# Kernel optimization log

Hardware: AMD Instinct MI355X
Metric: run time of the kernel (lower is better)

Reference implementation:

```python
import jax, jax.numpy as jnp
import numpy as np

N = 2_000_000
LAYER_DIMS = [6, 128, 48, 48, 48, 48, 48, 128, 3]  # 8 Linear layers


def setup_inputs() -> dict:
    key = jax.random.key(0)
    ks = jax.random.split(key, 2 + 2 * (len(LAYER_DIMS) - 1))
    inp = {
        "dimensions": jax.random.normal(ks[0], (N, 3), dtype=jnp.float32),
        "xyz": jax.random.normal(ks[1], (N, 3), dtype=jnp.float32),
    }
    # Kaiming-uniform-ish init like torch.nn.Linear defaults
    for i in range(len(LAYER_DIMS) - 1):
        fan_in, fan_out = LAYER_DIMS[i], LAYER_DIMS[i + 1]
        bound = 1.0 / np.sqrt(fan_in)
        inp[f"W{i+1}"] = jax.random.uniform(ks[2 + 2 * i], (fan_in, fan_out),
                                             minval=-bound, maxval=bound, dtype=jnp.float32)
        inp[f"b{i+1}"] = jax.random.uniform(ks[3 + 2 * i], (fan_out,),
                                             minval=-bound, maxval=bound, dtype=jnp.float32)
    return inp


def reference(dimensions, xyz,
              W1, b1, W2, b2, W3, b3, W4, b4,
              W5, b5, W6, b6, W7, b7, W8, b8) -> jnp.ndarray:
    x = jnp.concatenate([dimensions, xyz], axis=1)  # [N, 6]
    Ws = (W1, W2, W3, W4, W5, W6, W7)
    bs = (b1, b2, b3, b4, b5, b6, b7)
    for W, b in zip(Ws, bs):
        x = jax.nn.silu(x @ W + b)
    # final layer: Linear(128, 3) with Identity activation
    return x @ W8 + b8  # [N, 3]
```

## Files before the change

kernel.cpp:

```cpp
#include <hip/hip_runtime.h>

typedef __bf16 bf16x8 __attribute__((ext_vector_type(8)));
typedef __bf16 bf16x4 __attribute__((ext_vector_type(4)));
typedef float  f32x4  __attribute__((ext_vector_type(4)));

#define DEVFN static __device__ __forceinline__

DEVFN f32x4 mfma16(bf16x8 a, bf16x8 b, f32x4 c) {
  return __builtin_amdgcn_mfma_f32_16x16x32_bf16(a, b, c, 0, 0, 0);
}

DEVFN float silu_f(float x) {
  float e = __builtin_amdgcn_exp2f(x * -1.44269504f);
  return x * __builtin_amdgcn_rcpf(1.0f + e);
}

DEVFN void sbar() { __builtin_amdgcn_sched_barrier(0x7F); }

DEVFN bf16x8 bzero8() {
  bf16x8 v = {(__bf16)0.f,(__bf16)0.f,(__bf16)0.f,(__bf16)0.f,
              (__bf16)0.f,(__bf16)0.f,(__bf16)0.f,(__bf16)0.f};
  return v;
}
DEVFN f32x4 fzero4() { f32x4 v = {0.f,0.f,0.f,0.f}; return v; }

#define OFF_W2   0u
#define OFF_W3   12288u
#define OFF_W4   16896u
#define OFF_W5   21504u
#define OFF_W6   26112u
#define OFF_W7   30720u
#define OFF_BIAS 43008u
#define OFF_SCR  44992u
#define SCR_ROW    80u
#define SCR_RT     1280u
#define SCR_STRIDE 2560u
#define NWAVES   8
#define BLOCK    512
#define SMEM_TOTAL 65472u

DEVFN void init48(unsigned char* smem, unsigned base, const float* W, int Nout, int NT, int tid) {
  for (int t = tid; t < NT*512; t += BLOCK) {
    int i = t & 7, ln = (t >> 3) & 63, nt = t >> 9;
    int k = ((ln >> 4) << 3) + i;
    int n = (nt << 4) + (ln & 15);
    *(__bf16*)(smem + base + 2u*(unsigned)t) = (__bf16)W[k*Nout + n];
  }
  for (int t = tid; t < NT*256; t += BLOCK) {
    int i = t & 7, ln = (t >> 3) & 31, nt = t >> 8;
    int k = 32 + ((ln >> 4) << 3) + i;
    int n = (nt << 4) + (ln & 15);
    *(__bf16*)(smem + base + (unsigned)(NT*1024) + 2u*(unsigned)t) = (__bf16)W[k*Nout + n];
  }
}

DEVFN f32x4 biasFrag(const float* sB, int off, int nt, int g) {
  return *(const f32x4*)(sB + off + nt*16 + 4*g);
}

DEVFN void writeTile(unsigned char* sw, f32x4 t0, f32x4 t1, int slot, unsigned wBaseW) {
  bf16x4 p0, p1;
#pragma unroll
  for (int r = 0; r < 4; ++r) {
    p0[r] = (__bf16)silu_f(t0[r]);
    p1[r] = (__bf16)silu_f(t1[r]);
  }
  *(bf16x4*)(sw + wBaseW + (unsigned)slot*32u)           = p0;
  *(bf16x4*)(sw + SCR_RT + wBaseW + (unsigned)slot*32u)  = p1;
}

DEVFN void readA(const unsigned char* sw, unsigned aBase, bf16x8 (&af)[2]) {
  af[0] = *(const bf16x8*)(sw + aBase);
  af[1] = *(const bf16x8*)(sw + SCR_RT + aBase);
}

template<int NTO>
DEVFN void consumeFull(const unsigned char* smem, unsigned fragBase, unsigned bOff,
                       const bf16x8 (&af)[2], f32x4 (&acc)[2][NTO]) {
#pragma unroll
  for (int nt = 0; nt < NTO; ++nt) {
    bf16x8 w = *(const bf16x8*)(smem + fragBase + (unsigned)nt*1024u + bOff);
    acc[0][nt] = mfma16(w, af[0], acc[0][nt]);
    acc[1][nt] = mfma16(w, af[1], acc[1][nt]);
  }
}

template<int NTO>
DEVFN void consumeHalf(const unsigned char* smem, unsigned halfBase, unsigned hOff,
                       const bf16x8 (&af)[2], f32x4 (&acc)[2][NTO]) {
#pragma unroll
  for (int nt = 0; nt < NTO; ++nt) {
    bf16x8 w = *(const bf16x8*)(smem + halfBase + (unsigned)nt*512u + hOff);
    acc[0][nt] = mfma16(w, af[0], acc[0][nt]);
    acc[1][nt] = mfma16(w, af[1], acc[1][nt]);
  }
}

DEVFN void stream48(unsigned char* sw, unsigned char* smem,
                    unsigned wfragBase, const f32x4 (&accP)[2][3], f32x4 (&accO)[2][3],
                    unsigned wBaseW, unsigned aBase, unsigned bOff,
                    unsigned hOff, unsigned zOff) {
  bf16x8 af[2];
  sbar();
  writeTile(sw, accP[0][0], accP[1][0], 0, wBaseW);
  writeTile(sw, accP[0][1], accP[1][1], 1, wBaseW);
  sbar();
  readA(sw, aBase, af);
  consumeFull<3>(smem, wfragBase, bOff, af, accO);
  sbar();
  *(unsigned long long*)(sw + zOff)      = 0ull;
  *(unsigned long long*)(sw + zOff + 8u) = 0ull;
  writeTile(sw, accP[0][2], accP[1][2], 0, wBaseW);
  sbar();
  readA(sw, aBase, af);
  consumeHalf<3>(smem, wfragBase + 3u*1024u, hOff, af, accO);
}

DEVFN void loadIn(const float* __restrict__ dims, const float* __restrict__ xyz,
                  int grp, int lane, int N, float (&buf)[2][6]) {
#pragma unroll
  for (int rt = 0; rt < 2; ++rt)
#pragma unroll
    for (int j = 0; j < 6; ++j) buf[rt][j] = 0.f;
  if (lane < 16) {
#pragma unroll
    for (int rt = 0; rt < 2; ++rt) {
      int row = grp*32 + rt*16 + lane;
      if (row < N) {
        const float* dp = dims + (size_t)row*3u;
        const float* xp = xyz  + (size_t)row*3u;
        buf[rt][0] = dp[0]; buf[rt][1] = dp[1]; buf[rt][2] = dp[2];
        buf[rt][3] = xp[0]; buf[rt][4] = xp[1]; buf[rt][5] = xp[2];
      }
    }
  }
}

__global__ void __launch_bounds__(BLOCK, 4)
pinn_mlp_kernel(const float* __restrict__ dims, const float* __restrict__ xyz,
                const float* __restrict__ W1, const float* __restrict__ b1,
                const float* __restrict__ W2, const float* __restrict__ b2,
                const float* __restrict__ W3, const float* __restrict__ b3,
                const float* __restrict__ W4, const float* __restrict__ b4,
                const float* __restrict__ W5, const float* __restrict__ b5,
                const float* __restrict__ W6, const float* __restrict__ b6,
                const float* __restrict__ W7, const float* __restrict__ b7,
                const float* __restrict__ W8, const float* __restrict__ b8,
                float* __restrict__ out, int N) {
  __shared__ __align__(16) unsigned char smem[SMEM_TOTAL];
  const int tid  = threadIdx.x;
  const int lane = tid & 63;
  const int wave = tid >> 6;

  for (int t = tid; t < 6144; t += BLOCK) {
    int i = t & 7, ln = (t >> 3) & 63, f = t >> 9;
    int kt = f / 3, nt = f - kt*3;
    int k = kt*32 + ((ln >> 4) << 3) + i;
    int n = (nt << 4) + (ln & 15);
    *(__bf16*)(smem + OFF_W2 + 2u*(unsigned)t) = (__bf16)W2[k*48 + n];
  }
  init48(smem, OFF_W3, W3, 48, 3, tid);
  init48(smem, OFF_W4, W4, 48, 3, tid);
  init48(smem, OFF_W5, W5, 48, 3, tid);
  init48(smem, OFF_W6, W6, 48, 3, tid);
  init48(smem, OFF_W7, W7, 128, 8, tid);
  float* sB = (float*)(smem + OFF_BIAS);
  for (int t = tid; t < 496; t += BLOCK) {
    float v;
    if      (t < 128) v = b1[t];
    else if (t < 176) v = b2[t - 128];
    else if (t < 224) v = b3[t - 176];
    else if (t < 272) v = b4[t - 224];
    else if (t < 320) v = b5[t - 272];
    else if (t < 368) v = b6[t - 320];
    else              v = b7[t - 368];
    sB[t] = v;
  }

  bf16x8 w1f[8];
#pragma unroll
  for (int nt = 0; nt < 8; ++nt) w1f[nt] = bzero8();
  if (lane < 16) {
#pragma unroll
    for (int nt = 0; nt < 8; ++nt)
#pragma unroll
      for (int i = 0; i < 6; ++i)
        w1f[nt][i] = (__bf16)W1[i*128 + nt*16 + lane];
  }
  bf16x8 w8f[4];
#pragma unroll
  for (int kt = 0; kt < 4; ++kt) {
    w8f[kt] = bzero8();
    int n = lane & 15;
    if (n < 3) {
#pragma unroll
      for (int i = 0; i < 8; ++i) {
        int k = kt*32 + ((lane >> 4) << 3) + i;
        w8f[kt][i] = (__bf16)W8[k*3 + n];
      }
    }
  }

  __syncthreads();

  const int colId = lane & 15;
  const int g     = lane >> 4;
  unsigned char* sw = smem + OFF_SCR + (unsigned)wave * SCR_STRIDE;
  const unsigned aBase  = (unsigned)colId*SCR_ROW + (unsigned)g*16u;
  const unsigned wBaseW = (unsigned)colId*SCR_ROW + (unsigned)g*8u;
  const unsigned bOff   = (unsigned)lane*16u;
  const unsigned hOff   = (unsigned)(lane & 31)*16u;
  const unsigned zOff   = (unsigned)(lane >> 1)*SCR_ROW + 32u + (unsigned)(lane & 1)*16u;

  f32x4 b8v = fzero4();
  if (g == 0) { b8v[0] = b8[0]; b8v[1] = b8[1]; b8v[2] = b8[2]; }

  const int nGroups  = (N + 31) >> 5;
  const int gw0      = blockIdx.x*NWAVES + wave;
  const int gwStride = gridDim.x*NWAVES;

  float inC[2][6], inN[2][6];
  loadIn(dims, xyz, gw0, lane, N, inC);

  for (int grp = gw0; grp < nGroups; grp += gwStride) {
    const int base = grp * 32;

    bf16x8 a1[2] = {bzero8(), bzero8()};
    if (lane < 16) {
#pragma unroll
      for (int rt = 0; rt < 2; ++rt)
#pragma unroll
        for (int j = 0; j < 6; ++j) a1[rt][j] = (__bf16)inC[rt][j];
    }
    loadIn(dims, xyz, grp + gwStride, lane, N, inN);

    f32x4 accA[2][3], accB[2][3];
#pragma unroll
    for (int b = 0; b < 3; ++b) {
      f32x4 bi = biasFrag(sB, 128, b, g);
      accA[0][b] = bi; accA[1][b] = bi;
    }
#pragma unroll
    for (int kt = 0; kt < 4; ++kt) {
      sbar();
#pragma unroll
      for (int c = 0; c < 2; ++c) {
        int nt = 2*kt + c;
        f32x4 bi = biasFrag(sB, 0, nt, g);
        f32x4 t0 = mfma16(w1f[nt], a1[0], bi);
        f32x4 t1 = mfma16(w1f[nt], a1[1], bi);
        writeTile(sw, t0, t1, c, wBaseW);
      }
      sbar();
      bf16x8 af[2]; readA(sw, aBase, af);
      consumeFull<3>(smem, OFF_W2 + (unsigned)kt*3072u, bOff, af, accA);
    }

#pragma unroll
    for (int b = 0; b < 3; ++b) { f32x4 bi = biasFrag(sB, 176, b, g); accB[0][b] = bi; accB[1][b] = bi; }
    stream48(sw, smem, OFF_W3, accA, accB, wBaseW, aBase, bOff, hOff, zOff);
#pragma unroll
    for (int b = 0; b < 3; ++b) { f32x4 bi = biasFrag(sB, 224, b, g); accA[0][b] = bi; accA[1][b] = bi; }
    stream48(sw, smem, OFF_W4, accB, accA, wBaseW, aBase, bOff, hOff, zOff);
#pragma unroll
    for (int b = 0; b < 3; ++b) { f32x4 bi = biasFrag(sB, 272, b, g); accB[0][b] = bi; accB[1][b] = bi; }
    stream48(sw, smem, OFF_W5, accA, accB, wBaseW, aBase, bOff, hOff, zOff);
#pragma unroll
    for (int b = 0; b < 3; ++b) { f32x4 bi = biasFrag(sB, 320, b, g); accA[0][b] = bi; accA[1][b] = bi; }
    stream48(sw, smem, OFF_W6, accB, accA, wBaseW, aBase, bOff, hOff, zOff);

    sbar();
    writeTile(sw, accA[0][0], accA[1][0], 0, wBaseW);
    writeTile(sw, accA[0][1], accA[1][1], 1, wBaseW);
    sbar();
    bf16x8 af0[2]; readA(sw, aBase, af0);
    sbar();
    *(unsigned long long*)(sw + zOff)      = 0ull;
    *(unsigned long long*)(sw + zOff + 8u) = 0ull;
    writeTile(sw, accA[0][2], accA[1][2], 0, wBaseW);
    sbar();
    bf16x8 af1[2]; readA(sw, aBase, af1);

    f32x4 acc8[2] = {b8v, b8v};
#pragma unroll
    for (int kt = 0; kt < 4; ++kt) {
      sbar();
#pragma unroll
      for (int c = 0; c < 2; ++c) {
        int nt = 2*kt + c;
        bf16x8 wfull = *(const bf16x8*)(smem + OFF_W7 + (unsigned)nt*1024u + bOff);
        bf16x8 whalf = *(const bf16x8*)(smem + OFF_W7 + 8192u + (unsigned)nt*512u + hOff);
        f32x4 bi = biasFrag(sB, 368, nt, g);
        f32x4 t0 = mfma16(whalf, af1[0], mfma16(wfull, af0[0], bi));
        f32x4 t1 = mfma16(whalf, af1[1], mfma16(wfull, af0[1], bi));
        writeTile(sw, t0, t1, c, wBaseW);
      }
      sbar();
      bf16x8 af8[2]; readA(sw, aBase, af8);
      acc8[0] = mfma16(w8f[kt], af8[0], acc8[0]);
      acc8[1] = mfma16(w8f[kt], af8[1], acc8[1]);
    }

    if (g == 0) {
#pragma unroll
      for (int rt = 0; rt < 2; ++rt) {
        int row = base + rt*16 + colId;
        if (row < N) {
          size_t o = (size_t)row*3u;
          out[o+0] = acc8[rt][0];
          out[o+1] = acc8[rt][1];
          out[o+2] = acc8[rt][2];
        }
      }
    }

#pragma unroll
    for (int rt = 0; rt < 2; ++rt)
#pragma unroll
      for (int j = 0; j < 6; ++j) inC[rt][j] = inN[rt][j];
  }
}

extern "C" void kernel_launch(void* const* d_in, const int* in_sizes, int n_in,
                              void* d_out, int out_size, void* d_ws, size_t ws_size,
                              hipStream_t stream) {
  const float* dims = (const float*)d_in[0];
  const float* xyz  = (const float*)d_in[1];
  const float* W1 = (const float*)d_in[2];  const float* b1 = (const float*)d_in[3];
  const float* W2 = (const float*)d_in[4];  const float* b2 = (const float*)d_in[5];
  const float* W3 = (const float*)d_in[6];  const float* b3 = (const float*)d_in[7];
  const float* W4 = (const float*)d_in[8];  const float* b4 = (const float*)d_in[9];
  const float* W5 = (const float*)d_in[10]; const float* b5 = (const float*)d_in[11];
  const float* W6 = (const float*)d_in[12]; const float* b6 = (const float*)d_in[13];
  const float* W7 = (const float*)d_in[14]; const float* b7 = (const float*)d_in[15];
  const float* W8 = (const float*)d_in[16]; const float* b8 = (const float*)d_in[17];
  float* out = (float*)d_out;
  const int N = in_sizes[0] / 3;

  pinn_mlp_kernel<<<dim3(512), dim3(BLOCK), 0, stream>>>(
      dims, xyz, W1, b1, W2, b2, W3, b3, W4, b4, W5, b5, W6, b6, W7, b7, W8, b8,
      out, N);
}
```

Measured before the change: 298.2 us.

## Switch to 16x16x16 MFMA so layer outputs feed next layer in registers

Replaces the 16x16x32 bf16 MFMA with the 16x16x16 variant, whose output accumulator layout matches the B-operand layout. Each layer's silu output can then be packed directly into the next layer's input fragment without a round trip through per-wave LDS scratch. This removes the scratch buffer, its writes, reads, zero padding and scheduling barriers, and drops the 48-width padding to 64. In exchange it issues twice as many smaller MFMAs, each with half the K depth, and W1 now lives in LDS instead of registers.

```diff
diff --git a/kernel.cpp b/kernel.cpp
--- a/kernel.cpp
+++ b/kernel.cpp
@@ -1,13 +1,17 @@
 #include <hip/hip_runtime.h>
 
-typedef __bf16 bf16x8 __attribute__((ext_vector_type(8)));
 typedef __bf16 bf16x4 __attribute__((ext_vector_type(4)));
+typedef short  s16x4  __attribute__((ext_vector_type(4)));
 typedef float  f32x4  __attribute__((ext_vector_type(4)));
 
 #define DEVFN static __device__ __forceinline__
-
-DEVFN f32x4 mfma16(bf16x8 a, bf16x8 b, f32x4 c) {
-  return __builtin_amdgcn_mfma_f32_16x16x32_bf16(a, b, c, 0, 0, 0);
+#define BLOCK 512
+#define NWAVES 8
+
+DEVFN f32x4 mfma16(bf16x4 a, bf16x4 b, f32x4 c) {
+  s16x4 as = __builtin_bit_cast(s16x4, a);
+  s16x4 bs = __builtin_bit_cast(s16x4, b);
+  return __builtin_amdgcn_mfma_f32_16x16x16bf16_1k(as, bs, c, 0, 0, 0);
 }
 
 DEVFN float silu_f(float x) {
@@ -15,122 +19,88 @@
   return x * __builtin_amdgcn_rcpf(1.0f + e);
 }
 
-DEVFN void sbar() { __builtin_amdgcn_sched_barrier(0x7F); }
-
-DEVFN bf16x8 bzero8() {
-  bf16x8 v = {(__bf16)0.f,(__bf16)0.f,(__bf16)0.f,(__bf16)0.f,
-              (__bf16)0.f,(__bf16)0.f,(__bf16)0.f,(__bf16)0.f};
-  return v;
-}
-DEVFN f32x4 fzero4() { f32x4 v = {0.f,0.f,0.f,0.f}; return v; }
-
-#define OFF_W2   0u
-#define OFF_W3   12288u
-#define OFF_W4   16896u
-#define OFF_W5   21504u
-#define OFF_W6   26112u
-#define OFF_W7   30720u
-#define OFF_BIAS 43008u
-#define OFF_SCR  44992u
-#define SCR_ROW    80u
-#define SCR_RT     1280u
-#define SCR_STRIDE 2560u
-#define NWAVES   8
-#define BLOCK    512
-#define SMEM_TOTAL 65472u
-
-DEVFN void init48(unsigned char* smem, unsigned base, const float* W, int Nout, int NT, int tid) {
-  for (int t = tid; t < NT*512; t += BLOCK) {
-    int i = t & 7, ln = (t >> 3) & 63, nt = t >> 9;
-    int k = ((ln >> 4) << 3) + i;
-    int n = (nt << 4) + (ln & 15);
-    *(__bf16*)(smem + base + 2u*(unsigned)t) = (__bf16)W[k*Nout + n];
-  }
-  for (int t = tid; t < NT*256; t += BLOCK) {
-    int i = t & 7, ln = (t >> 3) & 31, nt = t >> 8;
-    int k = 32 + ((ln >> 4) << 3) + i;
-    int n = (nt << 4) + (ln & 15);
-    *(__bf16*)(smem + base + (unsigned)(NT*1024) + 2u*(unsigned)t) = (__bf16)W[k*Nout + n];
-  }
-}
-
-DEVFN f32x4 biasFrag(const float* sB, int off, int nt, int g) {
-  return *(const f32x4*)(sB + off + nt*16 + 4*g);
-}
-
-DEVFN void writeTile(unsigned char* sw, f32x4 t0, f32x4 t1, int slot, unsigned wBaseW) {
-  bf16x4 p0, p1;
-#pragma unroll
-  for (int r = 0; r < 4; ++r) {
-    p0[r] = (__bf16)silu_f(t0[r]);
-    p1[r] = (__bf16)silu_f(t1[r]);
-  }
-  *(bf16x4*)(sw + wBaseW + (unsigned)slot*32u)           = p0;
-  *(bf16x4*)(sw + SCR_RT + wBaseW + (unsigned)slot*32u)  = p1;
-}
-
-DEVFN void readA(const unsigned char* sw, unsigned aBase, bf16x8 (&af)[2]) {
-  af[0] = *(const bf16x8*)(sw + aBase);
-  af[1] = *(const bf16x8*)(sw + SCR_RT + aBase);
-}
-
-template<int NTO>
-DEVFN void consumeFull(const unsigned char* smem, unsigned fragBase, unsigned bOff,
-                       const bf16x8 (&af)[2], f32x4 (&acc)[2][NTO]) {
-#pragma unroll
-  for (int nt = 0; nt < NTO; ++nt) {
-    bf16x8 w = *(const bf16x8*)(smem + fragBase + (unsigned)nt*1024u + bOff);
-    acc[0][nt] = mfma16(w, af[0], acc[0][nt]);
-    acc[1][nt] = mfma16(w, af[1], acc[1][nt]);
-  }
-}
-
-template<int NTO>
-DEVFN void consumeHalf(const unsigned char* smem, unsigned halfBase, unsigned hOff,
-                       const bf16x8 (&af)[2], f32x4 (&acc)[2][NTO]) {
-#pragma unroll
-  for (int nt = 0; nt < NTO; ++nt) {
-    bf16x8 w = *(const bf16x8*)(smem + halfBase + (unsigned)nt*512u + hOff);
-    acc[0][nt] = mfma16(w, af[0], acc[0][nt]);
-    acc[1][nt] = mfma16(w, af[1], acc[1][nt]);
-  }
-}
-
-DEVFN void stream48(unsigned char* sw, unsigned char* smem,
-                    unsigned wfragBase, const f32x4 (&accP)[2][3], f32x4 (&accO)[2][3],
-                    unsigned wBaseW, unsigned aBase, unsigned bOff,
-                    unsigned hOff, unsigned zOff) {
-  bf16x8 af[2];
-  sbar();
-  writeTile(sw, accP[0][0], accP[1][0], 0, wBaseW);
-  writeTile(sw, accP[0][1], accP[1][1], 1, wBaseW);
-  sbar();
-  readA(sw, aBase, af);
-  consumeFull<3>(smem, wfragBase, bOff, af, accO);
-  sbar();
-  *(unsigned long long*)(sw + zOff)      = 0ull;
-  *(unsigned long long*)(sw + zOff + 8u) = 0ull;
-  writeTile(sw, accP[0][2], accP[1][2], 0, wBaseW);
-  sbar();
-  readA(sw, aBase, af);
-  consumeHalf<3>(smem, wfragBase + 3u*1024u, hOff, af, accO);
-}
-
-DEVFN void loadIn(const float* __restrict__ dims, const float* __restrict__ xyz,
-                  int grp, int lane, int N, float (&buf)[2][6]) {
-#pragma unroll
-  for (int rt = 0; rt < 2; ++rt)
-#pragma unroll
-    for (int j = 0; j < 6; ++j) buf[rt][j] = 0.f;
-  if (lane < 16) {
+DEVFN bf16x4 pksilu(f32x4 t) {
+  bf16x4 r;
+#pragma unroll
+  for (int j = 0; j < 4; ++j) r[j] = (__bf16)silu_f(t[j]);
+  return r;
+}
+
+#define OFF_W1   0u
+#define OFF_W2   4096u
+#define OFF_W3   16384u
+#define OFF_W4   20992u
+#define OFF_W5   25600u
+#define OFF_W6   30208u
+#define OFF_W7   34816u
+#define OFF_BIAS 47104u
+#define SMEM_TOTAL 49088u
+
+DEVFN void packW(unsigned char* smem, unsigned base, const float* W, int K, int N, int tid) {
+  int NT = N >> 4;
+  int total = (K >> 4) * NT * 256;
+  for (int t = tid; t < total; t += BLOCK) {
+    int i = t & 3, ln = (t >> 2) & 63, f = t >> 8;
+    int ks = f / NT, nt = f - ks * NT;
+    int k = 16 * ks + 4 * (ln >> 4) + i;
+    int n = 16 * nt + (ln & 15);
+    *(__bf16*)(smem + base + (unsigned)f * 512u + (unsigned)ln * 8u + (unsigned)i * 2u)
+        = (__bf16)W[k * N + n];
+  }
+}
+
+DEVFN f32x4 ldb(const float* sB, int off, int nt, int g) {
+  return *(const f32x4*)(sB + off + nt * 16 + 4 * g);
+}
+
+DEVFN bf16x4 ldw(const unsigned char* smem, unsigned addr) {
+  return *(const bf16x4*)(smem + addr);
+}
+
+DEVFN void layer33(const unsigned char* smem, unsigned wbase, const float* sB, int bOffL,
+                   unsigned wOff, int g, const bf16x4 (&xin)[2][3], bf16x4 (&xout)[2][3]) {
+  f32x4 acc[2][3];
+#pragma unroll
+  for (int nt = 0; nt < 3; ++nt) {
+    f32x4 bi = ldb(sB, bOffL, nt, g);
+    acc[0][nt] = bi; acc[1][nt] = bi;
+  }
+#pragma unroll
+  for (int ks = 0; ks < 3; ++ks)
+#pragma unroll
+    for (int nt = 0; nt < 3; ++nt) {
+      bf16x4 w = ldw(smem, wbase + (unsigned)(ks * 3 + nt) * 512u + wOff);
+      acc[0][nt] = mfma16(w, xin[0][ks], acc[0][nt]);
+      acc[1][nt] = mfma16(w, xin[1][ks], acc[1][nt]);
+    }
+#pragma unroll
+  for (int nt = 0; nt < 3; ++nt) {
+    xout[0][nt] = pksilu(acc[0][nt]);
+    xout[1][nt] = pksilu(acc[1][nt]);
+  }
+}
+
+DEVFN void loadIn6(const float* __restrict__ dims, const float* __restrict__ xyz,
+                   int grp, int g, int m, int N, float (&buf)[2][4]) {
+#pragma unroll
+  for (int rt = 0; rt < 2; ++rt) { buf[rt][0] = buf[rt][1] = buf[rt][2] = buf[rt][3] = 0.f; }
+  if (g == 0) {
 #pragma unroll
     for (int rt = 0; rt < 2; ++rt) {
-      int row = grp*32 + rt*16 + lane;
+      int row = grp * 32 + rt * 16 + m;
       if (row < N) {
-        const float* dp = dims + (size_t)row*3u;
-        const float* xp = xyz  + (size_t)row*3u;
+        const float* dp = dims + (size_t)row * 3u;
         buf[rt][0] = dp[0]; buf[rt][1] = dp[1]; buf[rt][2] = dp[2];
-        buf[rt][3] = xp[0]; buf[rt][4] = xp[1]; buf[rt][5] = xp[2];
+        buf[rt][3] = xyz[(size_t)row * 3u];
+      }
+    }
+  } else if (g == 1) {
+#pragma unroll
+    for (int rt = 0; rt < 2; ++rt) {
+      int row = grp * 32 + rt * 16 + m;
+      if (row < N) {
+        const float* xp = xyz + (size_t)row * 3u;
+        buf[rt][0] = xp[1]; buf[rt][1] = xp[2];
       }
     }
   }
@@ -151,20 +121,23 @@
   const int tid  = threadIdx.x;
   const int lane = tid & 63;
   const int wave = tid >> 6;
-
-  for (int t = tid; t < 6144; t += BLOCK) {
-    int i = t & 7, ln = (t >> 3) & 63, f = t >> 9;
-    int kt = f / 3, nt = f - kt*3;
-    int k = kt*32 + ((ln >> 4) << 3) + i;
-    int n = (nt << 4) + (ln & 15);
-    *(__bf16*)(smem + OFF_W2 + 2u*(unsigned)t) = (__bf16)W2[k*48 + n];
-  }
-  init48(smem, OFF_W3, W3, 48, 3, tid);
-  init48(smem, OFF_W4, W4, 48, 3, tid);
-  init48(smem, OFF_W5, W5, 48, 3, tid);
-  init48(smem, OFF_W6, W6, 48, 3, tid);
-  init48(smem, OFF_W7, W7, 128, 8, tid);
-  float* sB = (float*)(smem + OFF_BIAS);
+  const int m    = lane & 15;
+  const int g    = lane >> 4;
+
+  for (int t = tid; t < 2048; t += BLOCK) {
+    int i = t & 3, ln = (t >> 2) & 63, nt = t >> 8;
+    int k = 4 * (ln >> 4) + i;
+    int n = 16 * nt + (ln & 15);
+    float v = (k < 6) ? W1[k * 128 + n] : 0.f;
+    *(__bf16*)(smem + OFF_W1 + (unsigned)nt * 512u + (unsigned)ln * 8u + (unsigned)i * 2u) = (__bf16)v;
+  }
+  packW(smem, OFF_W2, W2, 128, 48, tid);
+  packW(smem, OFF_W3, W3, 48, 48, tid);
+  packW(smem, OFF_W4, W4, 48, 48, tid);
+  packW(smem, OFF_W5, W5, 48, 48, tid);
+  packW(smem, OFF_W6, W6, 48, 48, tid);
+  packW(smem, OFF_W7, W7, 48, 128, tid);
+  float* sBw = (float*)(smem + OFF_BIAS);
   for (int t = tid; t < 496; t += BLOCK) {
     float v;
     if      (t < 128) v = b1[t];
@@ -174,142 +147,124 @@
     else if (t < 320) v = b5[t - 272];
     else if (t < 368) v = b6[t - 320];
     else              v = b7[t - 368];
-    sB[t] = v;
-  }
-
-  bf16x8 w1f[8];
-#pragma unroll
-  for (int nt = 0; nt < 8; ++nt) w1f[nt] = bzero8();
-  if (lane < 16) {
-#pragma unroll
-    for (int nt = 0; nt < 8; ++nt)
-#pragma unroll
-      for (int i = 0; i < 6; ++i)
-        w1f[nt][i] = (__bf16)W1[i*128 + nt*16 + lane];
-  }
-  bf16x8 w8f[4];
-#pragma unroll
-  for (int kt = 0; kt < 4; ++kt) {
-    w8f[kt] = bzero8();
-    int n = lane & 15;
-    if (n < 3) {
-#pragma unroll
-      for (int i = 0; i < 8; ++i) {
-        int k = kt*32 + ((lane >> 4) << 3) + i;
-        w8f[kt][i] = (__bf16)W8[k*3 + n];
-      }
-    }
-  }
+    sBw[t] = v;
+  }
+
+  bf16x4 w8f[8];
+#pragma unroll
+  for (int ks = 0; ks < 8; ++ks) {
+    w8f[ks][0] = (__bf16)0.f; w8f[ks][1] = (__bf16)0.f;
+    w8f[ks][2] = (__bf16)0.f; w8f[ks][3] = (__bf16)0.f;
+    if (m < 3) {
+#pragma unroll
+      for (int i = 0; i < 4; ++i) {
+        int k = 16 * ks + 4 * g + i;
+        w8f[ks][i] = (__bf16)W8[k * 3 + m];
+      }
+    }
+  }
+  f32x4 b8v = {0.f, 0.f, 0.f, 0.f};
+  if (g == 0) { b8v[0] = b8[0]; b8v[1] = b8[1]; b8v[2] = b8[2]; }
 
   __syncthreads();
 
-  const int colId = lane & 15;
-  const int g     = lane >> 4;
-  unsigned char* sw = smem + OFF_SCR + (unsigned)wave * SCR_STRIDE;
-  const unsigned aBase  = (unsigned)colId*SCR_ROW + (unsigned)g*16u;
-  const unsigned wBaseW = (unsigned)colId*SCR_ROW + (unsigned)g*8u;
-  const unsigned bOff   = (unsigned)lane*16u;
-  const unsigned hOff   = (unsigned)(lane & 31)*16u;
-  const unsigned zOff   = (unsigned)(lane >> 1)*SCR_ROW + 32u + (unsigned)(lane & 1)*16u;
-
-  f32x4 b8v = fzero4();
-  if (g == 0) { b8v[0] = b8[0]; b8v[1] = b8[1]; b8v[2] = b8[2]; }
+  const float* sB = (const float*)(smem + OFF_BIAS);
+  const unsigned wOff = (unsigned)lane * 8u;
 
   const int nGroups  = (N + 31) >> 5;
-  const int gw0      = blockIdx.x*NWAVES + wave;
-  const int gwStride = gridDim.x*NWAVES;
-
-  float inC[2][6], inN[2][6];
-  loadIn(dims, xyz, gw0, lane, N, inC);
+  const int gw0      = blockIdx.x * NWAVES + wave;
+  const int gwStride = gridDim.x * NWAVES;
+
+  float inC[2][4], inN[2][4];
+  loadIn6(dims, xyz, gw0, g, m, N, inC);
 
   for (int grp = gw0; grp < nGroups; grp += gwStride) {
     const int base = grp * 32;
 
-    bf16x8 a1[2] = {bzero8(), bzero8()};
-    if (lane < 16) {
-#pragma unroll
-      for (int rt = 0; rt < 2; ++rt)
-#pragma unroll
-        for (int j = 0; j < 6; ++j) a1[rt][j] = (__bf16)inC[rt][j];
-    }
-    loadIn(dims, xyz, grp + gwStride, lane, N, inN);
-
-    f32x4 accA[2][3], accB[2][3];
-#pragma unroll
-    for (int b = 0; b < 3; ++b) {
-      f32x4 bi = biasFrag(sB, 128, b, g);
-      accA[0][b] = bi; accA[1][b] = bi;
-    }
-#pragma unroll
-    for (int kt = 0; kt < 4; ++kt) {
-      sbar();
-#pragma unroll
-      for (int c = 0; c < 2; ++c) {
-        int nt = 2*kt + c;
-        f32x4 bi = biasFrag(sB, 0, nt, g);
-        f32x4 t0 = mfma16(w1f[nt], a1[0], bi);
-        f32x4 t1 = mfma16(w1f[nt], a1[1], bi);
-        writeTile(sw, t0, t1, c, wBaseW);
-      }
-      sbar();
-      bf16x8 af[2]; readA(sw, aBase, af);
-      consumeFull<3>(smem, OFF_W2 + (unsigned)kt*3072u, bOff, af, accA);
-    }
-
-#pragma unroll
-    for (int b = 0; b < 3; ++b) { f32x4 bi = biasFrag(sB, 176, b, g); accB[0][b] = bi; accB[1][b] = bi; }
-    stream48(sw, smem, OFF_W3, accA, accB, wBaseW, aBase, bOff, hOff, zOff);
-#pragma unroll
-    for (int b = 0; b < 3; ++b) { f32x4 bi = biasFrag(sB, 224, b, g); accA[0][b] = bi; accA[1][b] = bi; }
-    stream48(sw, smem, OFF_W4, accB, accA, wBaseW, aBase, bOff, hOff, zOff);
-#pragma unroll
-    for (int b = 0; b < 3; ++b) { f32x4 bi = biasFrag(sB, 272, b, g); accB[0][b] = bi; accB[1][b] = bi; }
-    stream48(sw, smem, OFF_W5, accA, accB, wBaseW, aBase, bOff, hOff, zOff);
-#pragma unroll
-    for (int b = 0; b < 3; ++b) { f32x4 bi = biasFrag(sB, 320, b, g); accA[0][b] = bi; accA[1][b] = bi; }
-    stream48(sw, smem, OFF_W6, accB, accA, wBaseW, aBase, bOff, hOff, zOff);
-
-    sbar();
-    writeTile(sw, accA[0][0], accA[1][0], 0, wBaseW);
-    writeTile(sw, accA[0][1], accA[1][1], 1, wBaseW);
-    sbar();
-    bf16x8 af0[2]; readA(sw, aBase, af0);
-    sbar();
-    *(unsigned long long*)(sw + zOff)      = 0ull;
-    *(unsigned long long*)(sw + zOff + 8u) = 0ull;
-    writeTile(sw, accA[0][2], accA[1][2], 0, wBaseW);
-    sbar();
-    bf16x8 af1[2]; readA(sw, aBase, af1);
+    bf16x4 x1[2];
+#pragma unroll
+    for (int rt = 0; rt < 2; ++rt)
+#pragma unroll
+      for (int j = 0; j < 4; ++j) x1[rt][j] = (__bf16)inC[rt][j];
+    loadIn6(dims, xyz, grp + gwStride, g, m, N, inN);
+
+    f32x4 acc2[2][3];
+#pragma unroll
+    for (int nt = 0; nt < 3; ++nt) {
+      f32x4 bi = ldb(sB, 128, nt, g);
+      acc2[0][nt] = bi; acc2[1][nt] = bi;
+    }
+#pragma unroll
+    for (int h = 0; h < 2; ++h) {
+      bf16x4 x2h[2][4];
+#pragma unroll
+      for (int q = 0; q < 4; ++q) {
+        int nt = 4 * h + q;
+        f32x4 bi = ldb(sB, 0, nt, g);
+        bf16x4 w = ldw(smem, OFF_W1 + (unsigned)nt * 512u + wOff);
+        f32x4 t0 = mfma16(w, x1[0], bi);
+        f32x4 t1 = mfma16(w, x1[1], bi);
+        x2h[0][q] = pksilu(t0);
+        x2h[1][q] = pksilu(t1);
+      }
+#pragma unroll
+      for (int q = 0; q < 4; ++q) {
+        int ks = 4 * h + q;
+#pragma unroll
+        for (int nt = 0; nt < 3; ++nt) {
+          bf16x4 w = ldw(smem, OFF_W2 + (unsigned)(ks * 3 + nt) * 512u + wOff);
+          acc2[0][nt] = mfma16(w, x2h[0][q], acc2[0][nt]);
+          acc2[1][nt] = mfma16(w, x2h[1][q], acc2[1][nt]);
+        }
+      }
+    }
+    bf16x4 xa[2][3], xb[2][3];
+#pragma unroll
+    for (int nt = 0; nt < 3; ++nt) {
+      xa[0][nt] = pksilu(acc2[0][nt]);
+      xa[1][nt] = pksilu(acc2[1][nt]);
+    }
+
+    layer33(smem, OFF_W3, sB, 176, wOff, g, xa, xb);
+    layer33(smem, OFF_W4, sB, 224, wOff, g, xb, xa);
+    layer33(smem, OFF_W5, sB, 272, wOff, g, xa, xb);
+    layer33(smem, OFF_W6, sB, 320, wOff, g, xb, xa);
 
     f32x4 acc8[2] = {b8v, b8v};
 #pragma unroll
-    for (int kt = 0; kt < 4; ++kt) {
-      sbar();
-#pragma unroll
-      for (int c = 0; c < 2; ++c) {
-        int nt = 2*kt + c;
-        bf16x8 wfull = *(const bf16x8*)(smem + OFF_W7 + (unsigned)nt*1024u + bOff);
-        bf16x8 whalf = *(const bf16x8*)(smem + OFF_W7 + 8192u + (unsigned)nt*512u + hOff);
-        f32x4 bi = biasFrag(sB, 368, nt, g);
-        f32x4 t0 = mfma16(whalf, af1[0], mfma16(wfull, af0[0], bi));
-        f32x4 t1 = mfma16(whalf, af1[1], mfma16(wfull, af0[1], bi));
-        writeTile(sw, t0, t1, c, wBaseW);
-      }
-      sbar();
-      bf16x8 af8[2]; readA(sw, aBase, af8);
-      acc8[0] = mfma16(w8f[kt], af8[0], acc8[0]);
-      acc8[1] = mfma16(w8f[kt], af8[1], acc8[1]);
+    for (int h = 0; h < 2; ++h) {
+      f32x4 acc7[2][4];
+#pragma unroll
+      for (int q = 0; q < 4; ++q) {
+        f32x4 bi = ldb(sB, 368, 4 * h + q, g);
+        acc7[0][q] = bi; acc7[1][q] = bi;
+      }
+#pragma unroll
+      for (int ks = 0; ks < 3; ++ks)
+#pragma unroll
+        for (int q = 0; q < 4; ++q) {
+          bf16x4 w = ldw(smem, OFF_W7 + (unsigned)(ks * 8 + 4 * h + q) * 512u + wOff);
+          acc7[0][q] = mfma16(w, xa[0][ks], acc7[0][q]);
+          acc7[1][q] = mfma16(w, xa[1][ks], acc7[1][q]);
+        }
+#pragma unroll
+      for (int q = 0; q < 4; ++q) {
+        bf16x4 x7a = pksilu(acc7[0][q]);
+        bf16x4 x7b = pksilu(acc7[1][q]);
+        acc8[0] = mfma16(w8f[4 * h + q], x7a, acc8[0]);
+        acc8[1] = mfma16(w8f[4 * h + q], x7b, acc8[1]);
+      }
     }
 
     if (g == 0) {
 #pragma unroll
       for (int rt = 0; rt < 2; ++rt) {
-        int row = base + rt*16 + colId;
+        int row = base + rt * 16 + m;
         if (row < N) {
-          size_t o = (size_t)row*3u;
-          out[o+0] = acc8[rt][0];
-          out[o+1] = acc8[rt][1];
-          out[o+2] = acc8[rt][2];
+          size_t o = (size_t)row * 3u;
+          out[o + 0] = acc8[rt][0];
+          out[o + 1] = acc8[rt][1];
+          out[o + 2] = acc8[rt][2];
         }
       }
     }
@@ -317,7 +272,7 @@
 #pragma unroll
     for (int rt = 0; rt < 2; ++rt)
 #pragma unroll
-      for (int j = 0; j < 6; ++j) inC[rt][j] = inN[rt][j];
+      for (int j = 0; j < 4; ++j) inC[rt][j] = inN[rt][j];
   }
 }
 
```

Measured after the change: 886.9 us. 197% more time.
